# Kernel optimization log

Measured on AMD Instinct MI355X. Metric: run time of the kernel, lower is better.

## Reference

```python
import jax, jax.numpy as jnp
import numpy as np

H_SIZE = 1024
N_HEADS = 16
D_K = H_SIZE // N_HEADS


def setup_inputs() -> dict:
    key = jax.random.key(0)
    ks = jax.random.split(key, 12)
    s = 1.0 / np.sqrt(H_SIZE)
    inp = {
        "x": jax.random.normal(ks[0], (2, 2048, H_SIZE), dtype=jnp.float32),
        "Wq": jax.random.uniform(ks[1], (H_SIZE, H_SIZE), minval=-s, maxval=s),
        "bq": jax.random.uniform(ks[2], (H_SIZE,), minval=-s, maxval=s),
        "Wk": jax.random.uniform(ks[3], (H_SIZE, H_SIZE), minval=-s, maxval=s),
        "bk": jax.random.uniform(ks[4], (H_SIZE,), minval=-s, maxval=s),
        "Wv": jax.random.uniform(ks[5], (H_SIZE, H_SIZE), minval=-s, maxval=s),
        "bv": jax.random.uniform(ks[6], (H_SIZE,), minval=-s, maxval=s),
        "Wo": jax.random.uniform(ks[7], (H_SIZE, H_SIZE), minval=-s, maxval=s),
        "bo": jax.random.uniform(ks[8], (H_SIZE,), minval=-s, maxval=s),
        "ln_gamma": jnp.ones((H_SIZE,), dtype=jnp.float32),
        "ln_beta": jnp.zeros((H_SIZE,), dtype=jnp.float32),
    }
    return inp


def reference(x, Wq, bq, Wk, bk, Wv, bv, Wo, bo, ln_gamma, ln_beta):
    B, L, H = x.shape
    residual = x
    # QKV projections -> [B, n_heads, L, d_k]
    def proj(W, b):
        return (x @ W.T + b).reshape(B, L, N_HEADS, D_K).transpose(0, 2, 1, 3)
    q = proj(Wq, bq)
    k = proj(Wk, bk)
    v = proj(Wv, bv)
    # scaled dot-product attention (dropout = identity in eval mode)
    scores = jnp.einsum("bhqd,bhkd->bhqk", q, k) / jnp.sqrt(jnp.float32(D_K))
    attn = jax.nn.softmax(scores, axis=-1)
    out = jnp.einsum("bhqk,bhkd->bhqd", attn, v)
    out = out.transpose(0, 2, 1, 3).reshape(B, L, H)
    out = out @ Wo.T + bo
    # residual + LayerNorm
    y = out + residual
    mu = jnp.mean(y, axis=-1, keepdims=True)
    var = jnp.var(y, axis=-1, keepdims=True)
    y = (y - mu) / jnp.sqrt(var + 1e-5) * ln_gamma + ln_beta
    return y
```

## Files before the change

### kernel.cpp

```cpp
#include <hip/hip_runtime.h>

#define H_SIZE 1024
#define N_HEADS 16
#define D_K 64
#define SEQ 2048
#define BATCH 2
#define M_TOT 4096

typedef __bf16 __attribute__((ext_vector_type(8))) bf16_8;
typedef float __attribute__((ext_vector_type(4))) f32x4;
typedef float __attribute__((ext_vector_type(16))) f32x16;
typedef int __attribute__((ext_vector_type(4))) int4v;

#define SWZ(r) ((((r) & 7) ^ (((r) >> 3) & 7)))

__device__ __forceinline__ ushort f2bf(float f) {
    unsigned int u = __float_as_uint(f);
    unsigned int r = (u + 0x7FFFu + ((u >> 16) & 1u)) >> 16;
    return (ushort)r;
}

__device__ __forceinline__ unsigned int cvtpk(float lo, float hi) {
    unsigned int r;
    asm("v_cvt_pk_bf16_f32 %0, %1, %2" : "=v"(r) : "v"(lo), "v"(hi));
    return r;
}

__device__ __forceinline__ float exp2_raw(float x) {
    float r;
    asm("v_exp_f32 %0, %1" : "=v"(r) : "v"(x));
    return r;
}

__device__ __forceinline__ void gld16(void* lds, const void* g) {
    __builtin_amdgcn_global_load_lds(
        (const __attribute__((address_space(1))) unsigned int*)g,
        (__attribute__((address_space(3))) unsigned int*)lds, 16, 0, 0);
}

__global__ __launch_bounds__(256) void gemm_qkv(
    const float* __restrict__ X, const float* __restrict__ Wqf,
    const float* __restrict__ Wkf, const float* __restrict__ Wvf,
    const float* __restrict__ bq, const float* __restrict__ bk, const float* __restrict__ bv,
    ushort* __restrict__ Qb, ushort* __restrict__ Kb, ushort* __restrict__ Vtb) {
    constexpr int BK = 32;
    __shared__ ushort As[2][128 * BK];
    __shared__ ushort Bs[2][128 * BK];
    const int tid = threadIdx.x;
    const int lane = tid & 63, wid = tid >> 6;
    const int wr = wid >> 1, wc = wid & 1;
    const int hi = lane >> 4, lo = lane & 15;
    const int bm0 = blockIdx.x * 128;
    const int t3 = blockIdx.y >> 3;
    const int bn0 = (blockIdx.y & 7) * 128;
    const float* Bw = (t3 == 0) ? Wqf : (t3 == 1) ? Wkf : Wvf;
    const float* bias = (t3 == 0) ? bq : (t3 == 1) ? bk : bv;

    f32x4 acc[4][4] = {};

    const int srow = tid >> 2;
    const int c4 = tid & 3;
    const int pseg = (c4 ^ ((srow >> 1) & 3)) * 8;
    const float* gA0 = X + (size_t)(bm0 + srow) * H_SIZE + c4 * 8;
    const float* gA1 = gA0 + 64 * H_SIZE;
    const float* gB0 = Bw + (size_t)(bn0 + srow) * H_SIZE + c4 * 8;
    const float* gB1 = gB0 + 64 * H_SIZE;

    float4 ra0, ra1, ra2, ra3, rb0, rb1, rb2, rb3;

#define LOADREG(kt)                                        \
    {                                                      \
        ra0 = *(const float4*)(gA0 + (kt));                \
        ra1 = *(const float4*)(gA0 + (kt) + 4);            \
        ra2 = *(const float4*)(gA1 + (kt));                \
        ra3 = *(const float4*)(gA1 + (kt) + 4);            \
        rb0 = *(const float4*)(gB0 + (kt));                \
        rb1 = *(const float4*)(gB0 + (kt) + 4);            \
        rb2 = *(const float4*)(gB1 + (kt));                \
        rb3 = *(const float4*)(gB1 + (kt) + 4);            \
    }
#define CVTWRITE(bb)                                                           \
    {                                                                          \
        uint4 w;                                                               \
        w.x = cvtpk(ra0.x, ra0.y); w.y = cvtpk(ra0.z, ra0.w);                  \
        w.z = cvtpk(ra1.x, ra1.y); w.w = cvtpk(ra1.z, ra1.w);                  \
        *(uint4*)&As[bb][srow * BK + pseg] = w;                                \
        w.x = cvtpk(ra2.x, ra2.y); w.y = cvtpk(ra2.z, ra2.w);                  \
        w.z = cvtpk(ra3.x, ra3.y); w.w = cvtpk(ra3.z, ra3.w);                  \
        *(uint4*)&As[bb][(srow + 64) * BK + pseg] = w;                         \
        w.x = cvtpk(rb0.x, rb0.y); w.y = cvtpk(rb0.z, rb0.w);                  \
        w.z = cvtpk(rb1.x, rb1.y); w.w = cvtpk(rb1.z, rb1.w);                  \
        *(uint4*)&Bs[bb][srow * BK + pseg] = w;                                \
        w.x = cvtpk(rb2.x, rb2.y); w.y = cvtpk(rb2.z, rb2.w);                  \
        w.z = cvtpk(rb3.x, rb3.y); w.w = cvtpk(rb3.z, rb3.w);                  \
        *(uint4*)&Bs[bb][(srow + 64) * BK + pseg] = w;                         \
    }

    LOADREG(0);
    CVTWRITE(0);
    __syncthreads();

    constexpr int NT = H_SIZE / BK;
    const int rxv = (lo >> 1) & 3;
    for (int t = 0; t < NT; t++) {
        const int cur = t & 1;
        if (t + 1 < NT) LOADREG((t + 1) * BK);
        {
            bf16_8 af[4], bfv[4];
            const ushort* pa = &As[cur][(wr * 64 + lo) * BK + ((hi ^ rxv) * 8)];
            const ushort* pb = &Bs[cur][(wc * 64 + lo) * BK + ((hi ^ rxv) * 8)];
#pragma unroll
            for (int i = 0; i < 4; i++) af[i] = *(const bf16_8*)(pa + i * 16 * BK);
#pragma unroll
            for (int i = 0; i < 4; i++) bfv[i] = *(const bf16_8*)(pb + i * 16 * BK);
#pragma unroll
            for (int mi = 0; mi < 4; mi++)
#pragma unroll
                for (int ni = 0; ni < 4; ni++)
                    acc[mi][ni] = __builtin_amdgcn_mfma_f32_16x16x32_bf16(
                        af[mi], bfv[ni], acc[mi][ni], 0, 0, 0);
        }
        if (t + 1 < NT) {
            CVTWRITE(cur ^ 1);
            __syncthreads();
        }
    }
#undef LOADREG
#undef CVTWRITE

#pragma unroll
    for (int mi = 0; mi < 4; mi++) {
#pragma unroll
        for (int ni = 0; ni < 4; ni++) {
            const int row0 = bm0 + wr * 64 + mi * 16 + hi * 4;
            const int col = bn0 + wc * 64 + ni * 16 + lo;
            const float bv = bias[col];
            const int h = col >> 6, dk = col & 63;
            if (t3 == 2) {
                const int b = row0 >> 11, l0 = row0 & 2047;
                const int lsw0 = (l0 & ~63) | (((((l0 >> 3) & 7) ^ SWZ(dk)) & 7) << 3) | (l0 & 7);
                uint2 o;
                o.x = cvtpk(acc[mi][ni][0] + bv, acc[mi][ni][1] + bv);
                o.y = cvtpk(acc[mi][ni][2] + bv, acc[mi][ni][3] + bv);
                *(uint2*)&Vtb[((size_t)(b * N_HEADS + h) * D_K + dk) * SEQ + lsw0] = o;
            } else {
#pragma unroll
                for (int rr = 0; rr < 4; rr++) {
                    const int m = row0 + rr;
                    const int b = m >> 11, l = m & 2047;
                    float val = acc[mi][ni][rr] + bv;
                    if (t3 == 0) {
                        Qb[((size_t)(b * N_HEADS + h) * SEQ + l) * D_K + dk] =
                            f2bf(val * 0.18033688f);
                    } else {
                        int dks = ((((dk >> 3) ^ SWZ(l & 63)) & 7) << 3) | (dk & 7);
                        Kb[((size_t)(b * N_HEADS + h) * SEQ + l) * D_K + dks] = f2bf(val);
                    }
                }
            }
        }
    }
}

__global__ __launch_bounds__(256) void gemm_o(const ushort* __restrict__ A,
                                              const float* __restrict__ Wof,
                                              const float* __restrict__ bias,
                                              const float* __restrict__ resid,
                                              float* __restrict__ outp) {
    constexpr int BK = 32;
    __shared__ ushort As[2][128 * BK];
    __shared__ ushort Bs[2][64 * BK];
    const int tid = threadIdx.x;
    const int lane = tid & 63, wid = tid >> 6;
    const int wr = wid >> 1, wc = wid & 1;
    const int hi = lane >> 4, lo = lane & 15;
    const int bm0 = blockIdx.x * 128, bn0 = blockIdx.y * 64;

    f32x4 acc[4][2] = {};

    const int srow = tid >> 2;
    const int c4 = tid & 3;
    const int pseg = (c4 ^ ((srow >> 1) & 3)) * 8;
    const ushort* gA0 = A + (size_t)(bm0 + srow) * H_SIZE + c4 * 8;
    const ushort* gA1 = gA0 + 64 * H_SIZE;
    const float* gB0 = Wof + (size_t)(bn0 + srow) * H_SIZE + c4 * 8;

    uint4 wa0, wa1;
    float4 rb0, rb1;

#define LOADREG(kt)                                        \
    {                                                      \
        wa0 = *(const uint4*)(gA0 + (kt));                 \
        wa1 = *(const uint4*)(gA1 + (kt));                 \
        rb0 = *(const float4*)(gB0 + (kt));                \
        rb1 = *(const float4*)(gB0 + (kt) + 4);            \
    }
#define CVTWRITE(bb)                                                           \
    {                                                                          \
        *(uint4*)&As[bb][srow * BK + pseg] = wa0;                              \
        *(uint4*)&As[bb][(srow + 64) * BK + pseg] = wa1;                       \
        uint4 w;                                                               \
        w.x = cvtpk(rb0.x, rb0.y); w.y = cvtpk(rb0.z, rb0.w);                  \
        w.z = cvtpk(rb1.x, rb1.y); w.w = cvtpk(rb1.z, rb1.w);                  \
        *(uint4*)&Bs[bb][srow * BK + pseg] = w;                                \
    }

    LOADREG(0);
    CVTWRITE(0);
    __syncthreads();

    constexpr int NT = H_SIZE / BK;
    const int rxv = (lo >> 1) & 3;
    for (int t = 0; t < NT; t++) {
        const int cur = t & 1;
        if (t + 1 < NT) LOADREG((t + 1) * BK);
        {
            bf16_8 af[4], bfv[2];
            const ushort* pa = &As[cur][(wr * 64 + lo) * BK + ((hi ^ rxv) * 8)];
            const ushort* pb = &Bs[cur][(wc * 32 + lo) * BK + ((hi ^ rxv) * 8)];
#pragma unroll
            for (int i = 0; i < 4; i++) af[i] = *(const bf16_8*)(pa + i * 16 * BK);
#pragma unroll
            for (int i = 0; i < 2; i++) bfv[i] = *(const bf16_8*)(pb + i * 16 * BK);
#pragma unroll
            for (int mi = 0; mi < 4; mi++)
#pragma unroll
                for (int ni = 0; ni < 2; ni++)
                    acc[mi][ni] = __builtin_amdgcn_mfma_f32_16x16x32_bf16(
                        af[mi], bfv[ni], acc[mi][ni], 0, 0, 0);
        }
        if (t + 1 < NT) {
            CVTWRITE(cur ^ 1);
            __syncthreads();
        }
    }
#undef LOADREG
#undef CVTWRITE

#pragma unroll
    for (int mi = 0; mi < 4; mi++) {
#pragma unroll
        for (int ni = 0; ni < 2; ni++) {
            const int row0 = bm0 + wr * 64 + mi * 16 + hi * 4;
            const int col = bn0 + wc * 32 + ni * 16 + lo;
            const float bv = bias[col];
#pragma unroll
            for (int rr = 0; rr < 4; rr++) {
                const int m = row0 + rr;
                outp[(size_t)m * H_SIZE + col] =
                    acc[mi][ni][rr] + bv + resid[(size_t)m * H_SIZE + col];
            }
        }
    }
}

__global__ __launch_bounds__(256) void attn_kernel(const ushort* __restrict__ Q,
                                                   const ushort* __restrict__ Ksw,
                                                   const ushort* __restrict__ Vsw,
                                                   ushort* __restrict__ Out) {
    __shared__ ushort Ks[3][64 * 64];
    __shared__ ushort Vs[3][64 * 64];
    __shared__ float lsum_lds[4][32];
    const int lane = threadIdx.x & 63, wid = threadIdx.x >> 6;
    const int h32 = lane >> 5, q32 = lane & 31;

    const int lin = blockIdx.y * gridDim.x + blockIdx.x;
    const int nlin = (lin & 7) * 64 + (lin >> 3);
    const int bx = nlin & 15;
    const int bh = nlin >> 4;
    const int q0 = bx * 128 + wid * 32;
    const ushort* Qh = Q + (size_t)bh * SEQ * D_K;
    const ushort* Kp = Ksw + (size_t)bh * SEQ * D_K;
    const ushort* Vp = Vsw + (size_t)bh * D_K * SEQ;

    bf16_8 qf[4];
#pragma unroll
    for (int tt = 0; tt < 4; tt++)
        qf[tt] = *(const bf16_8*)(Qh + (size_t)(q0 + q32) * D_K + tt * 16 + h32 * 8);

    f32x16 oacc0 = {}, oacc1 = {};
    float ls = 0.f;

    const int koff = wid * 2048 + lane * 16;
    const int vrow = wid * 16 + (lane >> 3);
    const int vseg = (lane & 7) * 16;

#define STAGE(bb, kt)                                                             \
    {                                                                             \
        const char* kg = (const char*)(Kp + (size_t)(kt) * D_K);                  \
        char* kl = (char*)&Ks[bb][0];                                             \
        gld16(kl + koff, kg + koff);                                              \
        gld16(kl + koff + 1024, kg + koff + 1024);                                \
        char* vl = (char*)&Vs[bb][0];                                             \
        gld16(vl + vrow * 128 + vseg,                                             \
              (const char*)(Vp + (size_t)vrow * SEQ + (kt)) + vseg);              \
        gld16(vl + (vrow + 8) * 128 + vseg,                                       \
              (const char*)(Vp + (size_t)(vrow + 8) * SEQ + (kt)) + vseg);        \
    }

    STAGE(0, 0);
    STAGE(1, 64);
    asm volatile("s_waitcnt vmcnt(4)" ::: "memory");
    __builtin_amdgcn_s_barrier();
    __builtin_amdgcn_sched_barrier(0);

    constexpr int NTT = SEQ / 64;
    int cur = 0;
    for (int t = 0; t < NTT; t++) {
        int c2 = cur + 2; if (c2 >= 3) c2 -= 3;
        if (t + 2 < NTT) STAGE(c2, (t + 2) * 64);
        const ushort* kb = &Ks[cur][0];
        const ushort* vb = &Vs[cur][0];

        f32x16 st0 = {}, st1 = {};
        __builtin_amdgcn_s_setprio(1);
#pragma unroll
        for (int tt = 0; tt < 4; tt++) {
            const int krow = q32;
            int sg = (2 * tt + h32) ^ SWZ(krow);
            bf16_8 kf = *(const bf16_8*)(kb + krow * 64 + sg * 8);
            st0 = __builtin_amdgcn_mfma_f32_32x32x16_bf16(kf, qf[tt], st0, 0, 0, 0);
        }
#pragma unroll
        for (int tt = 0; tt < 4; tt++) {
            const int krow = 32 + q32;
            int sg = (2 * tt + h32) ^ SWZ(krow);
            bf16_8 kf = *(const bf16_8*)(kb + krow * 64 + sg * 8);
            st1 = __builtin_amdgcn_mfma_f32_32x32x16_bf16(kf, qf[tt], st1, 0, 0, 0);
        }
        __builtin_amdgcn_s_setprio(0);

        union { unsigned int w[4]; bf16_8 v; } pf00, pf01;
        float part0 = 0.f;
#pragma unroll
        for (int rr = 0; rr < 16; rr++) { st0[rr] = exp2_raw(st0[rr]); part0 += st0[rr]; }
#pragma unroll
        for (int i = 0; i < 2; i++) {
            unsigned int a = cvtpk(st0[2 * i], st0[2 * i + 1]);
            unsigned int b = cvtpk(st0[4 + 2 * i], st0[4 + 2 * i + 1]);
            asm volatile("v_permlane32_swap_b32 %0, %1" : "+v"(a), "+v"(b));
            pf00.w[i] = a; pf00.w[2 + i] = b;
            unsigned int c = cvtpk(st0[8 + 2 * i], st0[8 + 2 * i + 1]);
            unsigned int d = cvtpk(st0[12 + 2 * i], st0[12 + 2 * i + 1]);
            asm volatile("v_permlane32_swap_b32 %0, %1" : "+v"(c), "+v"(d));
            pf01.w[i] = c; pf01.w[2 + i] = d;
        }
        ls += part0 + __shfl_xor(part0, 32);

        __builtin_amdgcn_s_setprio(1);
        {
            const int vr0 = q32;
            int sg0 = (h32) ^ SWZ(vr0);
            int sg1 = (2 + h32) ^ SWZ(vr0);
            bf16_8 vf0 = *(const bf16_8*)(vb + vr0 * 64 + sg0 * 8);
            bf16_8 vf1 = *(const bf16_8*)(vb + vr0 * 64 + sg1 * 8);
            oacc0 = __builtin_amdgcn_mfma_f32_32x32x16_bf16(pf00.v, vf0, oacc0, 0, 0, 0);
            oacc0 = __builtin_amdgcn_mfma_f32_32x32x16_bf16(pf01.v, vf1, oacc0, 0, 0, 0);
            const int vr1 = 32 + q32;
            int sg2 = (h32) ^ SWZ(vr1);
            int sg3 = (2 + h32) ^ SWZ(vr1);
            bf16_8 vf2 = *(const bf16_8*)(vb + vr1 * 64 + sg2 * 8);
            bf16_8 vf3 = *(const bf16_8*)(vb + vr1 * 64 + sg3 * 8);
            oacc1 = __builtin_amdgcn_mfma_f32_32x32x16_bf16(pf00.v, vf2, oacc1, 0, 0, 0);
            oacc1 = __builtin_amdgcn_mfma_f32_32x32x16_bf16(pf01.v, vf3, oacc1, 0, 0, 0);
        }
        __builtin_amdgcn_s_setprio(0);

        union { unsigned int w[4]; bf16_8 v; } pf10, pf11;
        float part1 = 0.f;
#pragma unroll
        for (int rr = 0; rr < 16; rr++) { st1[rr] = exp2_raw(st1[rr]); part1 += st1[rr]; }
#pragma unroll
        for (int i = 0; i < 2; i++) {
            unsigned int a = cvtpk(st1[2 * i], st1[2 * i + 1]);
            unsigned int b = cvtpk(st1[4 + 2 * i], st1[4 + 2 * i + 1]);
            asm volatile("v_permlane32_swap_b32 %0, %1" : "+v"(a), "+v"(b));
            pf10.w[i] = a; pf10.w[2 + i] = b;
            unsigned int c = cvtpk(st1[8 + 2 * i], st1[8 + 2 * i + 1]);
            unsigned int d = cvtpk(st1[12 + 2 * i], st1[12 + 2 * i + 1]);
            asm volatile("v_permlane32_swap_b32 %0, %1" : "+v"(c), "+v"(d));
            pf11.w[i] = c; pf11.w[2 + i] = d;
        }
        ls += part1 + __shfl_xor(part1, 32);

        __builtin_amdgcn_s_setprio(1);
        {
            const int vr0 = q32;
            int sg0 = (4 + h32) ^ SWZ(vr0);
            int sg1 = (6 + h32) ^ SWZ(vr0);
            bf16_8 vf0 = *(const bf16_8*)(vb + vr0 * 64 + sg0 * 8);
            bf16_8 vf1 = *(const bf16_8*)(vb + vr0 * 64 + sg1 * 8);
            oacc0 = __builtin_amdgcn_mfma_f32_32x32x16_bf16(pf10.v, vf0, oacc0, 0, 0, 0);
            oacc0 = __builtin_amdgcn_mfma_f32_32x32x16_bf16(pf11.v, vf1, oacc0, 0, 0, 0);
            const int vr1 = 32 + q32;
            int sg2 = (4 + h32) ^ SWZ(vr1);
            int sg3 = (6 + h32) ^ SWZ(vr1);
            bf16_8 vf2 = *(const bf16_8*)(vb + vr1 * 64 + sg2 * 8);
            bf16_8 vf3 = *(const bf16_8*)(vb + vr1 * 64 + sg3 * 8);
            oacc1 = __builtin_amdgcn_mfma_f32_32x32x16_bf16(pf10.v, vf2, oacc1, 0, 0, 0);
            oacc1 = __builtin_amdgcn_mfma_f32_32x32x16_bf16(pf11.v, vf3, oacc1, 0, 0, 0);
        }
        __builtin_amdgcn_s_setprio(0);

        if (t + 1 < NTT) {
            if (t + 2 < NTT) { asm volatile("s_waitcnt vmcnt(4)" ::: "memory"); }
            else             { asm volatile("s_waitcnt vmcnt(0)" ::: "memory"); }
            __builtin_amdgcn_s_barrier();
            __builtin_amdgcn_sched_barrier(0);
        }
        cur = cur + 1; if (cur >= 3) cur -= 3;
    }
#undef STAGE

    if (lane < 32) lsum_lds[wid][q32] = 1.0f / ls;
    const int b = bh >> 4, h = bh & 15;
#pragma unroll
    for (int rr = 0; rr < 16; rr++) {
        const int qloc = (rr & 3) + 8 * (rr >> 2) + 4 * h32;
        const float inv = lsum_lds[wid][qloc];
        const int l = q0 + qloc;
        ushort* orow = Out + ((size_t)(b * SEQ + l)) * H_SIZE + h * 64;
        orow[q32] = f2bf(oacc0[rr] * inv);
        orow[32 + q32] = f2bf(oacc1[rr] * inv);
    }
}

__global__ __launch_bounds__(256) void ln_kernel(float* __restrict__ y,
                                                 const float* __restrict__ gamma,
                                                 const float* __restrict__ beta) {
    const int row = blockIdx.x;
    float4* p = (float4*)(y + (size_t)row * H_SIZE);
    float4 v = p[threadIdx.x];
    float s = v.x + v.y + v.z + v.w;
    float s2 = v.x * v.x + v.y * v.y + v.z * v.z + v.w * v.w;
#pragma unroll
    for (int off = 1; off < 64; off <<= 1) {
        s += __shfl_xor(s, off);
        s2 += __shfl_xor(s2, off);
    }
    __shared__ float ss[4], ss2[4];
    const int wid = threadIdx.x >> 6, lane = threadIdx.x & 63;
    if (lane == 0) { ss[wid] = s; ss2[wid] = s2; }
    __syncthreads();
    s = ss[0] + ss[1] + ss[2] + ss[3];
    s2 = ss2[0] + ss2[1] + ss2[2] + ss2[3];
    const float mean = s * (1.0f / H_SIZE);
    const float var = s2 * (1.0f / H_SIZE) - mean * mean;
    const float rstd = rsqrtf(var + 1e-5f);
    const float4 g = ((const float4*)gamma)[threadIdx.x];
    const float4 bt = ((const float4*)beta)[threadIdx.x];
    float4 o;
    o.x = (v.x - mean) * rstd * g.x + bt.x;
    o.y = (v.y - mean) * rstd * g.y + bt.y;
    o.z = (v.z - mean) * rstd * g.z + bt.z;
    o.w = (v.w - mean) * rstd * g.w + bt.w;
    p[threadIdx.x] = o;
}

extern "C" void kernel_launch(void* const* d_in, const int* in_sizes, int n_in,
                              void* d_out, int out_size, void* d_ws, size_t ws_size,
                              hipStream_t stream) {
    const float* x = (const float*)d_in[0];
    const float* Wq = (const float*)d_in[1];
    const float* bq = (const float*)d_in[2];
    const float* Wk = (const float*)d_in[3];
    const float* bk = (const float*)d_in[4];
    const float* Wv = (const float*)d_in[5];
    const float* bv = (const float*)d_in[6];
    const float* Wo = (const float*)d_in[7];
    const float* bo = (const float*)d_in[8];
    const float* gamma = (const float*)d_in[9];
    const float* beta = (const float*)d_in[10];

    char* ws = (char*)d_ws;
    ushort* Qb  = (ushort*)(ws + (16u << 20));
    ushort* Kb  = (ushort*)(ws + (24u << 20));
    ushort* Vtb = (ushort*)(ws + (32u << 20));
    ushort* Ao  = (ushort*)(ws + (40u << 20));

    dim3 gq(M_TOT / 128, 24);
    gemm_qkv<<<gq, 256, 0, stream>>>(x, Wq, Wk, Wv, bq, bk, bv, Qb, Kb, Vtb);

    dim3 g2(SEQ / 128, BATCH * N_HEADS);
    attn_kernel<<<g2, 256, 0, stream>>>(Qb, Kb, Vtb, Ao);

    dim3 go(M_TOT / 128, H_SIZE / 64);
    gemm_o<<<go, 256, 0, stream>>>(Ao, Wo, bo, x, (float*)d_out);

    ln_kernel<<<M_TOT, 256, 0, stream>>>((float*)d_out, gamma, beta);
}
```

Before: 132.4 us.

## Load K/V fragments directly from global memory instead of LDS triple-buffering

Removes the LDS triple-buffered staging of K and V tiles (global_load_lds with swizzle) in the attention kernel. Each wave now reads its MFMA operand fragments straight from global memory, and the swizzled K/V layouts in the QKV GEMM epilogue are dropped. This gets rid of block barriers and LDS traffic. In exchange, the four waves of a block no longer share K/V loads, so L2 traffic per block rises about fourfold. Load latency is also exposed inside the loop because there is no explicit prefetch.

```diff
diff --git a/kernel.cpp b/kernel.cpp
--- a/kernel.cpp
+++ b/kernel.cpp
@@ -12,8 +12,6 @@
 typedef float __attribute__((ext_vector_type(16))) f32x16;
 typedef int __attribute__((ext_vector_type(4))) int4v;
 
-#define SWZ(r) ((((r) & 7) ^ (((r) >> 3) & 7)))
-
 __device__ __forceinline__ ushort f2bf(float f) {
     unsigned int u = __float_as_uint(f);
     unsigned int r = (u + 0x7FFFu + ((u >> 16) & 1u)) >> 16;
@@ -30,12 +28,6 @@
     float r;
     asm("v_exp_f32 %0, %1" : "=v"(r) : "v"(x));
     return r;
-}
-
-__device__ __forceinline__ void gld16(void* lds, const void* g) {
-    __builtin_amdgcn_global_load_lds(
-        (const __attribute__((address_space(1))) unsigned int*)g,
-        (__attribute__((address_space(3))) unsigned int*)lds, 16, 0, 0);
 }
 
 __global__ __launch_bounds__(256) void gemm_qkv(
@@ -138,11 +130,10 @@
             const int h = col >> 6, dk = col & 63;
             if (t3 == 2) {
                 const int b = row0 >> 11, l0 = row0 & 2047;
-                const int lsw0 = (l0 & ~63) | (((((l0 >> 3) & 7) ^ SWZ(dk)) & 7) << 3) | (l0 & 7);
                 uint2 o;
                 o.x = cvtpk(acc[mi][ni][0] + bv, acc[mi][ni][1] + bv);
                 o.y = cvtpk(acc[mi][ni][2] + bv, acc[mi][ni][3] + bv);
-                *(uint2*)&Vtb[((size_t)(b * N_HEADS + h) * D_K + dk) * SEQ + lsw0] = o;
+                *(uint2*)&Vtb[((size_t)(b * N_HEADS + h) * D_K + dk) * SEQ + l0] = o;
             } else {
 #pragma unroll
                 for (int rr = 0; rr < 4; rr++) {
@@ -153,8 +144,7 @@
                         Qb[((size_t)(b * N_HEADS + h) * SEQ + l) * D_K + dk] =
                             f2bf(val * 0.18033688f);
                     } else {
-                        int dks = ((((dk >> 3) ^ SWZ(l & 63)) & 7) << 3) | (dk & 7);
-                        Kb[((size_t)(b * N_HEADS + h) * SEQ + l) * D_K + dks] = f2bf(val);
+                        Kb[((size_t)(b * N_HEADS + h) * SEQ + l) * D_K + dk] = f2bf(val);
                     }
                 }
             }
@@ -255,11 +245,9 @@
 }
 
 __global__ __launch_bounds__(256) void attn_kernel(const ushort* __restrict__ Q,
-                                                   const ushort* __restrict__ Ksw,
-                                                   const ushort* __restrict__ Vsw,
+                                                   const ushort* __restrict__ Kg,
+                                                   const ushort* __restrict__ Vg,
                                                    ushort* __restrict__ Out) {
-    __shared__ ushort Ks[3][64 * 64];
-    __shared__ ushort Vs[3][64 * 64];
     __shared__ float lsum_lds[4][32];
     const int lane = threadIdx.x & 63, wid = threadIdx.x >> 6;
     const int h32 = lane >> 5, q32 = lane & 31;
@@ -270,8 +258,6 @@
     const int bh = nlin >> 4;
     const int q0 = bx * 128 + wid * 32;
     const ushort* Qh = Q + (size_t)bh * SEQ * D_K;
-    const ushort* Kp = Ksw + (size_t)bh * SEQ * D_K;
-    const ushort* Vp = Vsw + (size_t)bh * D_K * SEQ;
 
     bf16_8 qf[4];
 #pragma unroll
@@ -281,53 +267,35 @@
     f32x16 oacc0 = {}, oacc1 = {};
     float ls = 0.f;
 
-    const int koff = wid * 2048 + lane * 16;
-    const int vrow = wid * 16 + (lane >> 3);
-    const int vseg = (lane & 7) * 16;
-
-#define STAGE(bb, kt)                                                             \
-    {                                                                             \
-        const char* kg = (const char*)(Kp + (size_t)(kt) * D_K);                  \
-        char* kl = (char*)&Ks[bb][0];                                             \
-        gld16(kl + koff, kg + koff);                                              \
-        gld16(kl + koff + 1024, kg + koff + 1024);                                \
-        char* vl = (char*)&Vs[bb][0];                                             \
-        gld16(vl + vrow * 128 + vseg,                                             \
-              (const char*)(Vp + (size_t)vrow * SEQ + (kt)) + vseg);              \
-        gld16(vl + (vrow + 8) * 128 + vseg,                                       \
-              (const char*)(Vp + (size_t)(vrow + 8) * SEQ + (kt)) + vseg);        \
-    }
-
-    STAGE(0, 0);
-    STAGE(1, 64);
-    asm volatile("s_waitcnt vmcnt(4)" ::: "memory");
-    __builtin_amdgcn_s_barrier();
-    __builtin_amdgcn_sched_barrier(0);
+    const ushort* kr0 = Kg + (size_t)bh * SEQ * D_K + (size_t)q32 * D_K + h32 * 8;
+    const ushort* kr1 = kr0 + 32 * D_K;
+    const ushort* vr0p = Vg + (size_t)bh * D_K * SEQ + (size_t)q32 * SEQ + h32 * 8;
+    const ushort* vr1p = vr0p + 32 * SEQ;
 
     constexpr int NTT = SEQ / 64;
-    int cur = 0;
     for (int t = 0; t < NTT; t++) {
-        int c2 = cur + 2; if (c2 >= 3) c2 -= 3;
-        if (t + 2 < NTT) STAGE(c2, (t + 2) * 64);
-        const ushort* kb = &Ks[cur][0];
-        const ushort* vb = &Vs[cur][0];
+        bf16_8 kf0[4], kf1[4], v0[4], v1[4];
+#pragma unroll
+        for (int tt = 0; tt < 4; tt++) {
+            kf0[tt] = *(const bf16_8*)(kr0 + tt * 16);
+            kf1[tt] = *(const bf16_8*)(kr1 + tt * 16);
+        }
+#pragma unroll
+        for (int j = 0; j < 4; j++) {
+            v0[j] = *(const bf16_8*)(vr0p + j * 16);
+            v1[j] = *(const bf16_8*)(vr1p + j * 16);
+        }
+        kr0 += 64 * D_K; kr1 += 64 * D_K;
+        vr0p += 64; vr1p += 64;
 
         f32x16 st0 = {}, st1 = {};
         __builtin_amdgcn_s_setprio(1);
 #pragma unroll
-        for (int tt = 0; tt < 4; tt++) {
-            const int krow = q32;
-            int sg = (2 * tt + h32) ^ SWZ(krow);
-            bf16_8 kf = *(const bf16_8*)(kb + krow * 64 + sg * 8);
-            st0 = __builtin_amdgcn_mfma_f32_32x32x16_bf16(kf, qf[tt], st0, 0, 0, 0);
-        }
-#pragma unroll
-        for (int tt = 0; tt < 4; tt++) {
-            const int krow = 32 + q32;
-            int sg = (2 * tt + h32) ^ SWZ(krow);
-            bf16_8 kf = *(const bf16_8*)(kb + krow * 64 + sg * 8);
-            st1 = __builtin_amdgcn_mfma_f32_32x32x16_bf16(kf, qf[tt], st1, 0, 0, 0);
-        }
+        for (int tt = 0; tt < 4; tt++)
+            st0 = __builtin_amdgcn_mfma_f32_32x32x16_bf16(kf0[tt], qf[tt], st0, 0, 0, 0);
+#pragma unroll
+        for (int tt = 0; tt < 4; tt++)
+            st1 = __builtin_amdgcn_mfma_f32_32x32x16_bf16(kf1[tt], qf[tt], st1, 0, 0, 0);
         __builtin_amdgcn_s_setprio(0);
 
         union { unsigned int w[4]; bf16_8 v; } pf00, pf01;
@@ -348,22 +316,10 @@
         ls += part0 + __shfl_xor(part0, 32);
 
         __builtin_amdgcn_s_setprio(1);
-        {
-            const int vr0 = q32;
-            int sg0 = (h32) ^ SWZ(vr0);
-            int sg1 = (2 + h32) ^ SWZ(vr0);
-            bf16_8 vf0 = *(const bf16_8*)(vb + vr0 * 64 + sg0 * 8);
-            bf16_8 vf1 = *(const bf16_8*)(vb + vr0 * 64 + sg1 * 8);
-            oacc0 = __builtin_amdgcn_mfma_f32_32x32x16_bf16(pf00.v, vf0, oacc0, 0, 0, 0);
-            oacc0 = __builtin_amdgcn_mfma_f32_32x32x16_bf16(pf01.v, vf1, oacc0, 0, 0, 0);
-            const int vr1 = 32 + q32;
-            int sg2 = (h32) ^ SWZ(vr1);
-            int sg3 = (2 + h32) ^ SWZ(vr1);
-            bf16_8 vf2 = *(const bf16_8*)(vb + vr1 * 64 + sg2 * 8);
-            bf16_8 vf3 = *(const bf16_8*)(vb + vr1 * 64 + sg3 * 8);
-            oacc1 = __builtin_amdgcn_mfma_f32_32x32x16_bf16(pf00.v, vf2, oacc1, 0, 0, 0);
-            oacc1 = __builtin_amdgcn_mfma_f32_32x32x16_bf16(pf01.v, vf3, oacc1, 0, 0, 0);
-        }
+        oacc0 = __builtin_amdgcn_mfma_f32_32x32x16_bf16(pf00.v, v0[0], oacc0, 0, 0, 0);
+        oacc0 = __builtin_amdgcn_mfma_f32_32x32x16_bf16(pf01.v, v0[1], oacc0, 0, 0, 0);
+        oacc1 = __builtin_amdgcn_mfma_f32_32x32x16_bf16(pf00.v, v1[0], oacc1, 0, 0, 0);
+        oacc1 = __builtin_amdgcn_mfma_f32_32x32x16_bf16(pf01.v, v1[1], oacc1, 0, 0, 0);
         __builtin_amdgcn_s_setprio(0);
 
         union { unsigned int w[4]; bf16_8 v; } pf10, pf11;
@@ -384,33 +340,12 @@
         ls += part1 + __shfl_xor(part1, 32);
 
         __builtin_amdgcn_s_setprio(1);
-        {
-            const int vr0 = q32;
-            int sg0 = (4 + h32) ^ SWZ(vr0);
-            int sg1 = (6 + h32) ^ SWZ(vr0);
-            bf16_8 vf0 = *(const bf16_8*)(vb + vr0 * 64 + sg0 * 8);
-            bf16_8 vf1 = *(const bf16_8*)(vb + vr0 * 64 + sg1 * 8);
-            oacc0 = __builtin_amdgcn_mfma_f32_32x32x16_bf16(pf10.v, vf0, oacc0, 0, 0, 0);
-            oacc0 = __builtin_amdgcn_mfma_f32_32x32x16_bf16(pf11.v, vf1, oacc0, 0, 0, 0);
-            const int vr1 = 32 + q32;
-            int sg2 = (4 + h32) ^ SWZ(vr1);
-            int sg3 = (6 + h32) ^ SWZ(vr1);
-            bf16_8 vf2 = *(const bf16_8*)(vb + vr1 * 64 + sg2 * 8);
-            bf16_8 vf3 = *(const bf16_8*)(vb + vr1 * 64 + sg3 * 8);
-            oacc1 = __builtin_amdgcn_mfma_f32_32x32x16_bf16(pf10.v, vf2, oacc1, 0, 0, 0);
-            oacc1 = __builtin_amdgcn_mfma_f32_32x32x16_bf16(pf11.v, vf3, oacc1, 0, 0, 0);
-        }
+        oacc0 = __builtin_amdgcn_mfma_f32_32x32x16_bf16(pf10.v, v0[2], oacc0, 0, 0, 0);
+        oacc0 = __builtin_amdgcn_mfma_f32_32x32x16_bf16(pf11.v, v0[3], oacc0, 0, 0, 0);
+        oacc1 = __builtin_amdgcn_mfma_f32_32x32x16_bf16(pf10.v, v1[2], oacc1, 0, 0, 0);
+        oacc1 = __builtin_amdgcn_mfma_f32_32x32x16_bf16(pf11.v, v1[3], oacc1, 0, 0, 0);
         __builtin_amdgcn_s_setprio(0);
-
-        if (t + 1 < NTT) {
-            if (t + 2 < NTT) { asm volatile("s_waitcnt vmcnt(4)" ::: "memory"); }
-            else             { asm volatile("s_waitcnt vmcnt(0)" ::: "memory"); }
-            __builtin_amdgcn_s_barrier();
-            __builtin_amdgcn_sched_barrier(0);
-        }
-        cur = cur + 1; if (cur >= 3) cur -= 3;
-    }
-#undef STAGE
+    }
 
     if (lane < 32) lsum_lds[wid][q32] = 1.0f / ls;
     const int b = bh >> 4, h = bh & 15;
```

New measurement: 194.0 us. 46.5% more time.
